# Kernel optimization log

Measured on AMD Instinct MI355X. Metric: run time of the kernel, lower is better.

The kernel has to match this reference:

```python
import jax, jax.numpy as jnp
import numpy as np

COMMITMENT_COST = 0.1


def setup_inputs() -> dict:
    key = jax.random.key(0)
    k1, k2 = jax.random.split(key)
    B, D, T, K = 8, 256, 2048, 8192
    z = jax.random.normal(k1, (B, D, T), dtype=jnp.float32)
    # nn.init.uniform_(weight, -1/dim, 1/dim)
    codebook = jax.random.uniform(k2, (K, D), dtype=jnp.float32,
                                  minval=-1.0 / D, maxval=1.0 / D)
    return {"z": z, "codebook": codebook}


def reference(z, codebook):
    B, D, T = z.shape
    # (B*T, D)
    z_flat = jnp.transpose(z, (0, 2, 1)).reshape(B * T, D)
    # squared euclidean distances to each codebook entry: (B*T, K)
    d = (jnp.sum(z_flat * z_flat, axis=1, keepdims=True)
         - 2.0 * (z_flat @ codebook.T)
         + jnp.sum(codebook * codebook, axis=1)[None, :])
    indices = jnp.argmin(d, axis=1)                      # (B*T,)
    z_q = codebook[indices].reshape(B, T, D)             # gather
    z_q = jnp.transpose(z_q, (0, 2, 1))                  # (B, D, T)

    codebook_loss = jnp.mean((z_q - jax.lax.stop_gradient(z)) ** 2)
    commitment_loss = COMMITMENT_COST * jnp.mean(
        (jax.lax.stop_gradient(z_q) - z) ** 2)
    loss = codebook_loss + commitment_loss

    # straight-through estimator
    z_q_st = z + jax.lax.stop_gradient(z_q - z)
    return z_q_st, indices.reshape(B, T), loss
```

## Files before the change

### kernel.cpp

```cpp
#include <hip/hip_runtime.h>
#include <hip/hip_bf16.h>
#include <float.h>
#include <math.h>

#define Bz 8
#define Dd 256
#define Tt 2048
#define Kk 8192
#define Mm (Bz*Tt)

#define NSPL 32

#define ZG_CAP 4096
#define PAIR_CAP 131072

#define RESCAN_MARGIN 6e-4f

typedef __attribute__((ext_vector_type(8))) _Float16 f16x8;
typedef __attribute__((ext_vector_type(4))) float    f32x4;

__device__ __forceinline__ void gld16(const void* g, void* l) {
  __builtin_amdgcn_global_load_lds(
      (const __attribute__((address_space(1))) void*)g,
      (__attribute__((address_space(3))) void*)l, 16, 0, 0);
}

__device__ __forceinline__ float np_sumsq128(const float* __restrict__ x) {
  float r0 = __fmul_rn(x[0], x[0]);
  float r1 = __fmul_rn(x[1], x[1]);
  float r2 = __fmul_rn(x[2], x[2]);
  float r3 = __fmul_rn(x[3], x[3]);
  float r4 = __fmul_rn(x[4], x[4]);
  float r5 = __fmul_rn(x[5], x[5]);
  float r6 = __fmul_rn(x[6], x[6]);
  float r7 = __fmul_rn(x[7], x[7]);
  for (int i = 8; i < 128; i += 8) {
    r0 = __fadd_rn(r0, __fmul_rn(x[i+0], x[i+0]));
    r1 = __fadd_rn(r1, __fmul_rn(x[i+1], x[i+1]));
    r2 = __fadd_rn(r2, __fmul_rn(x[i+2], x[i+2]));
    r3 = __fadd_rn(r3, __fmul_rn(x[i+3], x[i+3]));
    r4 = __fadd_rn(r4, __fmul_rn(x[i+4], x[i+4]));
    r5 = __fadd_rn(r5, __fmul_rn(x[i+5], x[i+5]));
    r6 = __fadd_rn(r6, __fmul_rn(x[i+6], x[i+6]));
    r7 = __fadd_rn(r7, __fmul_rn(x[i+7], x[i+7]));
  }
  return __fadd_rn(__fadd_rn(__fadd_rn(r0, r1), __fadd_rn(r2, r3)),
                   __fadd_rn(__fadd_rn(r4, r5), __fadd_rn(r6, r7)));
}
__device__ __forceinline__ float np_sumsq256(const float* __restrict__ x) {
  return __fadd_rn(np_sumsq128(x), np_sumsq128(x + 128));
}

__global__ void k_pre(const float* __restrict__ z, const float* __restrict__ cb,
                      _Float16* __restrict__ Ah, _Float16* __restrict__ Bh,
                      float* __restrict__ sc,
                      double* __restrict__ loss_accum, int* __restrict__ rc) {
  const int bid = blockIdx.x;
  const int tid = threadIdx.x;
  if (bid < 1024) {
    __shared__ _Float16 tile[64][64 + 8];
    const int b  = bid >> 7;
    const int dt = (bid >> 5) & 3;
    const int tt = bid & 31;
    const int d0 = dt * 64, t0 = tt * 64;
    const float* zb = z + ((size_t)b * Dd + d0) * Tt + t0;
    #pragma unroll
    for (int p = 0; p < 4; ++p) {
      const int d  = p * 16 + (tid >> 4);
      const int tl = (tid & 15) * 4;
      const float4 v = *(const float4*)(zb + (size_t)d * Tt + tl);
      tile[tl+0][d] = (_Float16)v.x;
      tile[tl+1][d] = (_Float16)v.y;
      tile[tl+2][d] = (_Float16)v.z;
      tile[tl+3][d] = (_Float16)v.w;
    }
    __syncthreads();
    const int r = tid >> 2, seg = tid & 3;
    const int m = b * Tt + t0 + r;
    int4* dst = (int4*)(Ah + (size_t)m * Dd + d0 + seg * 16);
    const int4* srcv = (const int4*)(&tile[r][seg * 16]);
    dst[0] = srcv[0];
    dst[1] = srcv[1];
  } else if (bid < 2048) {
    const size_t g = (size_t)(bid - 1024) * 256 + tid;
    const float4 v0 = *(const float4*)(cb + g * 8);
    const float4 v1 = *(const float4*)(cb + g * 8 + 4);
    f16x8 o;
    o[0] = (_Float16)(v0.x * 256.f); o[1] = (_Float16)(v0.y * 256.f);
    o[2] = (_Float16)(v0.z * 256.f); o[3] = (_Float16)(v0.w * 256.f);
    o[4] = (_Float16)(v1.x * 256.f); o[5] = (_Float16)(v1.y * 256.f);
    o[6] = (_Float16)(v1.z * 256.f); o[7] = (_Float16)(v1.w * 256.f);
    *(f16x8*)(Bh + g * 8) = o;
  } else {
    if (bid == 2048 && tid == 0) {
      *loss_accum = 0.0; rc[0] = 0; rc[1] = 0; rc[2] = 0;
    }
    const int gid = (bid - 2048) * 256 + tid;
    const int lane = gid & 63;
    const int j = lane & 7, sub = lane >> 3;
    const int row = (gid >> 6) * 8 + sub;
    if (row >= Kk) return;
    const float* x = cb + (size_t)row * Dd;
    float c0 = __fmul_rn(x[j], x[j]);
    float c1 = __fmul_rn(x[128 + j], x[128 + j]);
    #pragma unroll
    for (int i = 8; i < 128; i += 8) {
      c0 = __fadd_rn(c0, __fmul_rn(x[j + i], x[j + i]));
      c1 = __fadd_rn(c1, __fmul_rn(x[128 + j + i], x[128 + j + i]));
    }
    #pragma unroll
    for (int off = 1; off <= 4; off <<= 1) {
      c0 = __fadd_rn(c0, __shfl_xor(c0, off));
      c1 = __fadd_rn(c1, __shfl_xor(c1, off));
    }
    if (j == 0) sc[row] = __fadd_rn(c0, c1);
  }
}

__global__ __launch_bounds__(512, 4)
void k_mfma(const _Float16* __restrict__ Ah, const _Float16* __restrict__ Bh,
            const float* __restrict__ sc,
            float* __restrict__ pd1, float* __restrict__ pd2, int* __restrict__ pi1) {
  __shared__ __align__(16) _Float16 As[128 * 64];
  __shared__ __align__(16) _Float16 Bs[256 * 64];
  __shared__ float mr1[512];
  __shared__ float mr2[512];
  __shared__ int   mri[512];

  const int tid  = threadIdx.x;
  const int bx   = blockIdx.x & 31;
  const int by   = blockIdx.x >> 5;
  const int m0   = by * 128, n0 = bx * 256;
  const int w    = tid >> 6, lane = tid & 63;
  const int wy   = w >> 2, wx = w & 3;
  const int l15  = lane & 15, quad = lane >> 4;
  const int lhi  = lane >> 3, llo = lane & 7;
  const int p    = llo ^ lhi;
  const int sw   = l15 & 7;

  f32x4 acc[4][4];
  #pragma unroll
  for (int mi = 0; mi < 4; ++mi)
    #pragma unroll
    for (int ni = 0; ni < 4; ++ni)
      acc[mi][ni] = (f32x4){0.f, 0.f, 0.f, 0.f};

  for (int kc = 0; kc < 4; ++kc) {
    __syncthreads();
    #pragma unroll
    for (int i = 0; i < 2; ++i) {
      const int c  = w * 2 + i;
      const int r8 = c * 8 + lhi;
      gld16(Ah + (size_t)(m0 + r8) * Dd + kc * 64 + p * 8, As + c * 512);
    }
    #pragma unroll
    for (int i = 0; i < 4; ++i) {
      const int c  = w * 4 + i;
      const int r8 = c * 8 + lhi;
      gld16(Bh + (size_t)(n0 + r8) * Dd + kc * 64 + p * 8, Bs + c * 512);
    }
    __syncthreads();
    #pragma unroll
    for (int ks = 0; ks < 2; ++ks) {
      f16x8 af[4], bf[4];
      #pragma unroll
      for (int mi = 0; mi < 4; ++mi)
        af[mi] = *(const f16x8*)(As + (wy*64 + mi*16 + l15) * 64 + (((ks*4 + quad) ^ sw) * 8));
      #pragma unroll
      for (int ni = 0; ni < 4; ++ni)
        bf[ni] = *(const f16x8*)(Bs + (wx*64 + ni*16 + l15) * 64 + (((ks*4 + quad) ^ sw) * 8));
      #pragma unroll
      for (int mi = 0; mi < 4; ++mi)
        #pragma unroll
        for (int ni = 0; ni < 4; ++ni)
          acc[mi][ni] = __builtin_amdgcn_mfma_f32_16x16x32_f16(bf[ni], af[mi], acc[mi][ni], 0, 0, 0);
    }
  }

  float scv[4][4];
  #pragma unroll
  for (int ni = 0; ni < 4; ++ni)
    *(float4*)&scv[ni][0] = *(const float4*)(sc + n0 + wx * 64 + ni * 16 + quad * 4);

  float s1[4], s2[4]; int i1[4];
  #pragma unroll
  for (int mi = 0; mi < 4; ++mi) {
    float a1 = INFINITY, a2 = INFINITY; int ai = 0x7fffffff;
    #pragma unroll
    for (int ni = 0; ni < 4; ++ni)
      #pragma unroll
      for (int r = 0; r < 4; ++r) {
        const float sv = fmaf(-0.0078125f, acc[mi][ni][r], scv[ni][r]);
        const int   k  = n0 + wx * 64 + ni * 16 + quad * 4 + r;
        if (sv < a1) { a2 = a1; a1 = sv; ai = k; }
        else if (sv < a2) a2 = sv;
      }
    s1[mi] = a1; s2[mi] = a2; i1[mi] = ai;
  }

  #pragma unroll
  for (int off = 16; off <= 32; off <<= 1)
    #pragma unroll
    for (int q = 0; q < 4; ++q) {
      const float o1 = __shfl_xor(s1[q], off);
      const float o2 = __shfl_xor(s2[q], off);
      const int   oi = __shfl_xor(i1[q], off);
      const float n2 = fminf(fminf(s2[q], o2), fmaxf(s1[q], o1));
      if (o1 < s1[q] || (o1 == s1[q] && oi < i1[q])) { s1[q] = o1; i1[q] = oi; }
      s2[q] = n2;
    }

  if (quad == 0) {
    #pragma unroll
    for (int mi = 0; mi < 4; ++mi) {
      const int ml = wy * 64 + mi * 16 + l15;
      mr1[ml * 4 + wx] = s1[mi];
      mr2[ml * 4 + wx] = s2[mi];
      mri[ml * 4 + wx] = i1[mi];
    }
  }
  __syncthreads();
  if (tid < 128) {
    float a1 = INFINITY, a2 = INFINITY; int ai = 0x7fffffff;
    #pragma unroll
    for (int x = 0; x < 4; ++x) {
      const float b1 = mr1[tid * 4 + x], b2 = mr2[tid * 4 + x];
      const int   bi = mri[tid * 4 + x];
      if (b1 < a1 || (b1 == a1 && bi < ai)) { a2 = fminf(a1, b2); a1 = b1; ai = bi; }
      else a2 = fminf(a2, b1);
    }
    const size_t o = (size_t)bx * Mm + (size_t)(m0 + tid);
    pd1[o] = a1; pd2[o] = a2; pi1[o] = ai;
  }
}

__global__ void k_combine(const float* __restrict__ pd1, const float* __restrict__ pd2,
                          const int* __restrict__ pi1, int* __restrict__ idxf,
                          int* __restrict__ rc, int* __restrict__ rlist,
                          int* __restrict__ pairs, int* __restrict__ slist,
                          float* __restrict__ outIdx) {
  const int m = blockIdx.x * blockDim.x + threadIdx.x;
  if (m >= Mm) return;
  float a1 = INFINITY, a2 = INFINITY; int ai = 0x7fffffff;
  for (int spl = 0; spl < NSPL; ++spl) {
    const size_t o = (size_t)spl * Mm + m;
    const float b1 = pd1[o], b2 = pd2[o]; const int bi = pi1[o];
    if (b1 < a1 || (b1 == a1 && bi < ai)) { a2 = fminf(a1, b2); a1 = b1; ai = bi; }
    else a2 = fminf(a2, b1);
  }
  idxf[m]   = ai;
  outIdx[m] = (float)ai;
  if (a2 - a1 <= RESCAN_MARGIN) {
    const int p = atomicAdd(&rc[0], 1);
    if (p < ZG_CAP) {
      rlist[p] = m;
      const float thr = a1 + RESCAN_MARGIN;
      int nc = 0;
      for (int spl = 0; spl < NSPL; ++spl) {
        const size_t o = (size_t)spl * Mm + m;
        if (pd2[o] <= thr) nc += 256;
        else if (pd1[o] <= thr) ++nc;
      }
      const int base = atomicAdd(&rc[1], nc);
      if (base + nc <= PAIR_CAP) {
        int wp = base;
        for (int spl = 0; spl < NSPL; ++spl) {
          const size_t o = (size_t)spl * Mm + m;
          const float b1 = pd1[o], b2 = pd2[o];
          if (b2 <= thr) {
            const int k0 = spl * 256;
            for (int c = 0; c < 256; ++c) pairs[wp++] = (p << 13) | (k0 + c);
          } else if (b1 <= thr) {
            pairs[wp++] = (p << 13) | pi1[o];
          }
        }
      } else {
        for (int q = base; q < PAIR_CAP; ++q) pairs[q] = -1;
        const int s = atomicAdd(&rc[2], 1); slist[s] = m;
      }
    } else {
      const int s = atomicAdd(&rc[2], 1); slist[s] = m;
    }
  }
}

__global__ void k_gather(const float* __restrict__ z, const int* __restrict__ rc,
                         const int* __restrict__ rlist, float* __restrict__ zg,
                         float* __restrict__ Ag, unsigned long long* __restrict__ pbrow) {
  __shared__ float zr[Dd];
  const int cnt = min(rc[0], ZG_CAP);
  for (int it = blockIdx.x; it < cnt; it += gridDim.x) {
    const int m = rlist[it];
    const int b = m / Tt, t = m & (Tt - 1);
    __syncthreads();
    zr[threadIdx.x] = z[(size_t)b * Dd * Tt + (size_t)threadIdx.x * Tt + t];
    __syncthreads();
    zg[(size_t)it * Dd + threadIdx.x] = zr[threadIdx.x];
    if (threadIdx.x == 0) { Ag[it] = np_sumsq256(zr); pbrow[it] = ~0ull; }
  }
}

__global__ __launch_bounds__(256)
void k_rescan_pairs(const float* __restrict__ cb, const float* __restrict__ sc,
                    const int* __restrict__ rc, const float* __restrict__ zg,
                    const float* __restrict__ Ag,
                    const int* __restrict__ pairs,
                    unsigned long long* __restrict__ pbrow) {
  const int n = min(rc[1], PAIR_CAP);
  const int i = blockIdx.x * 256 + threadIdx.x;
  if (i >= n) return;
  const int pr = pairs[i];
  if (pr < 0) return;
  const int it = pr >> 13, k = pr & (Kk - 1);
  const float* __restrict__ zp = zg + (size_t)it * Dd;
  const float* __restrict__ cp = cb + (size_t)k * Dd;
  double M8 = 0.0;
  #pragma unroll
  for (int sg = 0; sg < 8; ++sg) {
    double a0 = 0.0, a1 = 0.0, a2 = 0.0, a3 = 0.0;
    #pragma unroll
    for (int j = 0; j < 32; j += 4) {
      const float4 c4 = *(const float4*)(cp + sg * 32 + j);
      const float4 z4 = *(const float4*)(zp + sg * 32 + j);
      a0 = fma((double)c4.x, (double)z4.x, a0);
      a1 = fma((double)c4.y, (double)z4.y, a1);
      a2 = fma((double)c4.z, (double)z4.z, a2);
      a3 = fma((double)c4.w, (double)z4.w, a3);
    }
    M8 += (a0 + a1) + (a2 + a3);
  }
  const float M  = (float)M8;
  const float t1 = __fsub_rn(Ag[it], __fmul_rn(2.0f, M));
  const float dq = __fadd_rn(t1, sc[k]);
  unsigned int fb = __float_as_uint(dq);
  fb = (fb & 0x80000000u) ? ~fb : (fb | 0x80000000u);
  const unsigned long long pack = ((unsigned long long)fb << 32) | (unsigned)k;
  atomicMin(pbrow + it, pack);
}

__global__ void k_rescan_final(const int* __restrict__ rc, const int* __restrict__ rlist,
                               const unsigned long long* __restrict__ pbrow,
                               int* __restrict__ idxf, float* __restrict__ outIdx) {
  const int cnt = min(rc[0], ZG_CAP);
  const int it = blockIdx.x * blockDim.x + threadIdx.x;
  if (it < cnt) {
    const unsigned long long pb = pbrow[it];
    if (pb != ~0ull) {
      const int idx = (int)(unsigned)(pb & 0xFFFFFFFFull);
      const int m = rlist[it];
      idxf[m] = idx; outIdx[m] = (float)idx;
    }
  }
}

__global__ void k_rescan_slow(const float* __restrict__ z, const float* __restrict__ cb,
                              const float* __restrict__ sc,
                              const int* __restrict__ rc, const int* __restrict__ slist,
                              int* __restrict__ idxf, float* __restrict__ outIdx) {
  __shared__ float zrow[Dd];
  __shared__ float Ash;
  __shared__ float sval[256];
  __shared__ int   sidx[256];
  const int tid = threadIdx.x;
  const int cnt = rc[2];
  for (int it = blockIdx.x; it < cnt; it += gridDim.x) {
    const int m = slist[it];
    const int b = m / Tt, t = m & (Tt - 1);
    __syncthreads();
    zrow[tid] = z[(size_t)b * Dd * Tt + (size_t)tid * Tt + t];
    __syncthreads();
    if (tid == 0) Ash = np_sumsq256(zrow);
    __syncthreads();
    const float A = Ash;
    float best = INFINITY; int bi = 0x7fffffff;
    for (int k = tid; k < Kk; k += 256) {
      const float* cr = cb + (size_t)k * Dd;
      double a0 = 0.0, a1 = 0.0, a2 = 0.0, a3 = 0.0;
      for (int d = 0; d < Dd; d += 4) {
        const float4 c4 = *(const float4*)(cr + d);
        a0 = fma((double)c4.x, (double)zrow[d+0], a0);
        a1 = fma((double)c4.y, (double)zrow[d+1], a1);
        a2 = fma((double)c4.z, (double)zrow[d+2], a2);
        a3 = fma((double)c4.w, (double)zrow[d+3], a3);
      }
      const float M  = (float)((a0 + a1) + (a2 + a3));
      const float t1 = __fsub_rn(A, __fmul_rn(2.0f, M));
      const float dq = __fadd_rn(t1, sc[k]);
      if (dq < best) { best = dq; bi = k; }
    }
    sval[tid] = best; sidx[tid] = bi;
    __syncthreads();
    for (int off = 128; off; off >>= 1) {
      if (tid < off) {
        if (sval[tid+off] < sval[tid] ||
            (sval[tid+off] == sval[tid] && sidx[tid+off] < sidx[tid])) {
          sval[tid] = sval[tid+off]; sidx[tid] = sidx[tid+off];
        }
      }
      __syncthreads();
    }
    if (tid == 0) { idxf[m] = sidx[0]; outIdx[m] = (float)sidx[0]; }
    __syncthreads();
  }
}

__global__ void k_out(const float* __restrict__ z, const float* __restrict__ cb,
                      const int* __restrict__ idxf,
                      float* __restrict__ outZ, double* __restrict__ loss_accum) {
  __shared__ float tile[64][65];
  const int tid = threadIdx.x;
  const int bidx = blockIdx.x;
  const int b  = bidx >> 7;
  const int dt = (bidx >> 5) & 3;
  const int tt = bidx & 31;
  const int d0 = dt * 64, t0 = tt * 64;
  {
    const int r = tid >> 2, seg = tid & 3;
    const int idx = idxf[b * Tt + t0 + r];
    const float* src = cb + (size_t)idx * Dd + d0 + seg * 16;
    #pragma unroll
    for (int q4 = 0; q4 < 4; ++q4) {
      const float4 v = *(const float4*)(src + q4 * 4);
      tile[seg * 16 + q4 * 4 + 0][r] = v.x;
      tile[seg * 16 + q4 * 4 + 1][r] = v.y;
      tile[seg * 16 + q4 * 4 + 2][r] = v.z;
      tile[seg * 16 + q4 * 4 + 3][r] = v.w;
    }
  }
  __syncthreads();
  const float* zbase = z + ((size_t)b * Dd + d0) * Tt + t0;
  float*       obase = outZ + ((size_t)b * Dd + d0) * Tt + t0;
  double ls = 0.0;
  #pragma unroll
  for (int p = 0; p < 4; ++p) {
    const int d  = p * 16 + (tid >> 4);
    const int t4 = (tid & 15) * 4;
    const float4 zv = *(const float4*)(zbase + (size_t)d * Tt + t4);
    const float q0 = tile[d][t4+0], q1 = tile[d][t4+1];
    const float q2 = tile[d][t4+2], q3 = tile[d][t4+3];
    const float r0 = q0 - zv.x, r1 = q1 - zv.y, r2 = q2 - zv.z, r3 = q3 - zv.w;
    float4 o;
    o.x = zv.x + r0; o.y = zv.y + r1; o.z = zv.z + r2; o.w = zv.w + r3;
    *(float4*)(obase + (size_t)d * Tt + t4) = o;
    ls += (double)r0*r0 + (double)r1*r1 + (double)r2*r2 + (double)r3*r3;
  }
  #pragma unroll
  for (int off = 32; off; off >>= 1) ls += __shfl_down(ls, off);
  if ((tid & 63) == 0) atomicAdd(loss_accum, ls);
}

__global__ void k_finalize(const double* __restrict__ loss_accum, float* __restrict__ outLoss) {
  const double mean = *loss_accum / (double)((size_t)Bz * Dd * Tt);
  *outLoss = (float)(mean + 0.1 * mean);
}

extern "C" void kernel_launch(void* const* d_in, const int* in_sizes, int n_in,
                              void* d_out, int out_size, void* d_ws, size_t ws_size,
                              hipStream_t stream) {
  (void)in_sizes; (void)n_in; (void)out_size; (void)ws_size;
  const float* z  = (const float*)d_in[0];
  const float* cb = (const float*)d_in[1];

  float* outZ    = (float*)d_out;
  float* outIdx  = outZ + (size_t)Bz * Dd * Tt;
  float* outLoss = outIdx + Mm;

  char* w = (char*)d_ws;
  double*    loss_accum = (double*)w;    w += 16;
  int*       rc         = (int*)w;       w += 16;
  int*       rlist      = (int*)w;       w += sizeof(int)   * Mm;
  int*       slist      = (int*)w;       w += sizeof(int)   * Mm;
  int*       idxf       = (int*)w;       w += sizeof(int)   * Mm;
  float*     sc         = (float*)w;     w += sizeof(float) * Kk;
  _Float16*  Ah         = (_Float16*)w;  w += sizeof(_Float16) * (size_t)Mm * Dd;
  _Float16*  Bh         = (_Float16*)w;  w += sizeof(_Float16) * (size_t)Kk * Dd;
  float*     zg         = (float*)w;     w += sizeof(float) * (size_t)ZG_CAP * Dd;
  float*     Ag         = (float*)w;     w += sizeof(float) * ZG_CAP;
  unsigned long long* pbrow = (unsigned long long*)w; w += sizeof(unsigned long long) * ZG_CAP;
  int*       pairs      = (int*)w;       w += sizeof(int) * PAIR_CAP;
  float*     pd1        = (float*)w;     w += sizeof(float) * (size_t)NSPL * Mm;
  float*     pd2        = (float*)w;     w += sizeof(float) * (size_t)NSPL * Mm;
  int*       pi1        = (int*)w;

  k_pre         <<<dim3(2304), 256, 0, stream>>>(z, cb, Ah, Bh, sc, loss_accum, rc);
  k_mfma        <<<dim3((Mm / 128) * (Kk / 256)), 512, 0, stream>>>(Ah, Bh, sc, pd1, pd2, pi1);
  k_combine     <<<dim3(Mm / 256), 256, 0, stream>>>(pd1, pd2, pi1, idxf, rc, rlist, pairs, slist, outIdx);
  k_gather      <<<dim3(256), 256, 0, stream>>>(z, rc, rlist, zg, Ag, pbrow);
  k_rescan_pairs<<<dim3(PAIR_CAP / 256), 256, 0, stream>>>(cb, sc, rc, zg, Ag, pairs, pbrow);
  k_rescan_slow <<<dim3(64), 256, 0, stream>>>(z, cb, sc, rc, slist, idxf, outIdx);
  k_rescan_final<<<dim3(ZG_CAP / 256), 256, 0, stream>>>(rc, rlist, pbrow, idxf, outIdx);
  k_out         <<<dim3(1024), 256, 0, stream>>>(z, cb, idxf, outZ, loss_accum);
  k_finalize    <<<dim3(1), 1, 0, stream>>>(loss_accum, outLoss);
}
```

Before: 293.4 us.

## Replace global pair list with per-row wave rescan and fold final fixup into output

Drops the serial per-thread pair-list construction in the combine kernel, which wrote up to 256 pairs per ambiguous row. Each wave now rebuilds its row's candidate list from the per-split partials using ballots and rescans those candidates directly. The separate final-fixup kernel is removed, and the output kernel reads the packed rescan minimum through a per-row position map. The combine kernel now launches 64-thread blocks with its loop unrolled, and the gather kernel computes the squared norm with 8 lanes plus shuffles instead of a single thread.

```diff
diff --git a/kernel.cpp b/kernel.cpp
--- a/kernel.cpp
+++ b/kernel.cpp
@@ -12,7 +12,6 @@
 #define NSPL 32
 
 #define ZG_CAP 4096
-#define PAIR_CAP 131072
 
 #define RESCAN_MARGIN 6e-4f
 
@@ -237,11 +236,12 @@
 __global__ void k_combine(const float* __restrict__ pd1, const float* __restrict__ pd2,
                           const int* __restrict__ pi1, int* __restrict__ idxf,
                           int* __restrict__ rc, int* __restrict__ rlist,
-                          int* __restrict__ pairs, int* __restrict__ slist,
-                          float* __restrict__ outIdx) {
-  const int m = blockIdx.x * blockDim.x + threadIdx.x;
+                          float* __restrict__ rthr, int* __restrict__ posm,
+                          int* __restrict__ slist, float* __restrict__ outIdx) {
+  const int m = blockIdx.x * 64 + threadIdx.x;
   if (m >= Mm) return;
   float a1 = INFINITY, a2 = INFINITY; int ai = 0x7fffffff;
+  #pragma unroll
   for (int spl = 0; spl < NSPL; ++spl) {
     const size_t o = (size_t)spl * Mm + m;
     const float b1 = pd1[o], b2 = pd2[o]; const int bi = pi1[o];
@@ -250,38 +250,18 @@
   }
   idxf[m]   = ai;
   outIdx[m] = (float)ai;
+  int pos = -1;
   if (a2 - a1 <= RESCAN_MARGIN) {
     const int p = atomicAdd(&rc[0], 1);
     if (p < ZG_CAP) {
       rlist[p] = m;
-      const float thr = a1 + RESCAN_MARGIN;
-      int nc = 0;
-      for (int spl = 0; spl < NSPL; ++spl) {
-        const size_t o = (size_t)spl * Mm + m;
-        if (pd2[o] <= thr) nc += 256;
-        else if (pd1[o] <= thr) ++nc;
-      }
-      const int base = atomicAdd(&rc[1], nc);
-      if (base + nc <= PAIR_CAP) {
-        int wp = base;
-        for (int spl = 0; spl < NSPL; ++spl) {
-          const size_t o = (size_t)spl * Mm + m;
-          const float b1 = pd1[o], b2 = pd2[o];
-          if (b2 <= thr) {
-            const int k0 = spl * 256;
-            for (int c = 0; c < 256; ++c) pairs[wp++] = (p << 13) | (k0 + c);
-          } else if (b1 <= thr) {
-            pairs[wp++] = (p << 13) | pi1[o];
-          }
-        }
-      } else {
-        for (int q = base; q < PAIR_CAP; ++q) pairs[q] = -1;
-        const int s = atomicAdd(&rc[2], 1); slist[s] = m;
-      }
+      rthr[p]  = a1 + RESCAN_MARGIN;
+      pos = p;
     } else {
       const int s = atomicAdd(&rc[2], 1); slist[s] = m;
     }
   }
+  posm[m] = pos;
 }
 
 __global__ void k_gather(const float* __restrict__ z, const int* __restrict__ rc,
@@ -289,30 +269,38 @@
                          float* __restrict__ Ag, unsigned long long* __restrict__ pbrow) {
   __shared__ float zr[Dd];
   const int cnt = min(rc[0], ZG_CAP);
+  const int tid = threadIdx.x;
   for (int it = blockIdx.x; it < cnt; it += gridDim.x) {
     const int m = rlist[it];
     const int b = m / Tt, t = m & (Tt - 1);
     __syncthreads();
-    zr[threadIdx.x] = z[(size_t)b * Dd * Tt + (size_t)threadIdx.x * Tt + t];
-    __syncthreads();
-    zg[(size_t)it * Dd + threadIdx.x] = zr[threadIdx.x];
-    if (threadIdx.x == 0) { Ag[it] = np_sumsq256(zr); pbrow[it] = ~0ull; }
-  }
-}
-
-__global__ __launch_bounds__(256)
-void k_rescan_pairs(const float* __restrict__ cb, const float* __restrict__ sc,
-                    const int* __restrict__ rc, const float* __restrict__ zg,
-                    const float* __restrict__ Ag,
-                    const int* __restrict__ pairs,
-                    unsigned long long* __restrict__ pbrow) {
-  const int n = min(rc[1], PAIR_CAP);
-  const int i = blockIdx.x * 256 + threadIdx.x;
-  if (i >= n) return;
-  const int pr = pairs[i];
-  if (pr < 0) return;
-  const int it = pr >> 13, k = pr & (Kk - 1);
-  const float* __restrict__ zp = zg + (size_t)it * Dd;
+    zr[tid] = z[(size_t)b * Dd * Tt + (size_t)tid * Tt + t];
+    __syncthreads();
+    zg[(size_t)it * Dd + tid] = zr[tid];
+    if (tid < 8) {
+      const int j = tid;
+      float c0 = __fmul_rn(zr[j], zr[j]);
+      float c1 = __fmul_rn(zr[128 + j], zr[128 + j]);
+      #pragma unroll
+      for (int i = 8; i < 128; i += 8) {
+        c0 = __fadd_rn(c0, __fmul_rn(zr[j + i], zr[j + i]));
+        c1 = __fadd_rn(c1, __fmul_rn(zr[128 + j + i], zr[128 + j + i]));
+      }
+      #pragma unroll
+      for (int off = 1; off <= 4; off <<= 1) {
+        c0 = __fadd_rn(c0, __shfl_xor(c0, off));
+        c1 = __fadd_rn(c1, __shfl_xor(c1, off));
+      }
+      if (j == 0) { Ag[it] = __fadd_rn(c0, c1); pbrow[it] = ~0ull; }
+    }
+  }
+}
+
+__device__ __forceinline__ void rescan_cand(const float* __restrict__ cb,
+                                            const float* __restrict__ sc,
+                                            const float* __restrict__ zp,
+                                            const float Az, const int k,
+                                            unsigned long long* __restrict__ pb) {
   const float* __restrict__ cp = cb + (size_t)k * Dd;
   double M8 = 0.0;
   #pragma unroll
@@ -330,26 +318,55 @@
     M8 += (a0 + a1) + (a2 + a3);
   }
   const float M  = (float)M8;
-  const float t1 = __fsub_rn(Ag[it], __fmul_rn(2.0f, M));
+  const float t1 = __fsub_rn(Az, __fmul_rn(2.0f, M));
   const float dq = __fadd_rn(t1, sc[k]);
   unsigned int fb = __float_as_uint(dq);
   fb = (fb & 0x80000000u) ? ~fb : (fb | 0x80000000u);
   const unsigned long long pack = ((unsigned long long)fb << 32) | (unsigned)k;
-  atomicMin(pbrow + it, pack);
-}
-
-__global__ void k_rescan_final(const int* __restrict__ rc, const int* __restrict__ rlist,
-                               const unsigned long long* __restrict__ pbrow,
-                               int* __restrict__ idxf, float* __restrict__ outIdx) {
-  const int cnt = min(rc[0], ZG_CAP);
-  const int it = blockIdx.x * blockDim.x + threadIdx.x;
-  if (it < cnt) {
-    const unsigned long long pb = pbrow[it];
-    if (pb != ~0ull) {
-      const int idx = (int)(unsigned)(pb & 0xFFFFFFFFull);
-      const int m = rlist[it];
-      idxf[m] = idx; outIdx[m] = (float)idx;
-    }
+  atomicMin(pb, pack);
+}
+
+__global__ __launch_bounds__(256)
+void k_rescan_rows(const float* __restrict__ cb, const float* __restrict__ sc,
+                   const int* __restrict__ rc, const int* __restrict__ rlist,
+                   const float* __restrict__ rthr,
+                   const float* __restrict__ pd1, const float* __restrict__ pd2,
+                   const int* __restrict__ pi1,
+                   const float* __restrict__ zg, const float* __restrict__ Ag,
+                   unsigned long long* __restrict__ pbrow) {
+  __shared__ int clist[4][32];
+  const int cnt  = min(rc[0], ZG_CAP);
+  const int wv   = threadIdx.x >> 6;
+  const int lane = threadIdx.x & 63;
+  const int it   = blockIdx.x * 4 + wv;
+  if (it >= cnt) return;
+  const int   m   = rlist[it];
+  const float thr = rthr[it];
+  const float Az  = Ag[it];
+  const float* __restrict__ zp = zg + (size_t)it * Dd;
+
+  int  cand = -1;
+  bool dump = false;
+  if (lane < NSPL) {
+    const size_t o = (size_t)lane * Mm + m;
+    const float b1 = pd1[o], b2 = pd2[o];
+    if (b2 <= thr) dump = true;
+    else if (b1 <= thr) cand = pi1[o];
+  }
+  const unsigned long long m1 = __ballot(cand >= 0);
+  unsigned long long m2 = __ballot(dump);
+  if (cand >= 0)
+    clist[wv][__popcll(m1 & ((1ull << lane) - 1))] = cand;
+  asm volatile("s_waitcnt lgkmcnt(0)" ::: "memory");
+  __builtin_amdgcn_sched_barrier(0);
+  const int ns = __popcll(m1);
+  if (lane < ns)
+    rescan_cand(cb, sc, zp, Az, clist[wv][lane], pbrow + it);
+  while (m2) {
+    const int s = (int)(__ffsll((long long)m2) - 1); m2 &= m2 - 1;
+    #pragma unroll
+    for (int rr = 0; rr < 4; ++rr)
+      rescan_cand(cb, sc, zp, Az, s * 256 + rr * 64 + lane, pbrow + it);
   }
 }
 
@@ -405,8 +422,10 @@
 }
 
 __global__ void k_out(const float* __restrict__ z, const float* __restrict__ cb,
-                      const int* __restrict__ idxf,
-                      float* __restrict__ outZ, double* __restrict__ loss_accum) {
+                      const int* __restrict__ idxf, const int* __restrict__ posm,
+                      const unsigned long long* __restrict__ pbrow,
+                      float* __restrict__ outZ, float* __restrict__ outIdx,
+                      double* __restrict__ loss_accum) {
   __shared__ float tile[64][65];
   const int tid = threadIdx.x;
   const int bidx = blockIdx.x;
@@ -416,7 +435,16 @@
   const int d0 = dt * 64, t0 = tt * 64;
   {
     const int r = tid >> 2, seg = tid & 3;
-    const int idx = idxf[b * Tt + t0 + r];
+    const int m = b * Tt + t0 + r;
+    int idx = idxf[m];
+    const int pos = posm[m];
+    if (pos >= 0) {
+      const unsigned long long pb = pbrow[pos];
+      if (pb != ~0ull) {
+        idx = (int)(unsigned)(pb & 0xFFFFFFFFull);
+        if (seg == 0) outIdx[m] = (float)idx;
+      }
+    }
     const float* src = cb + (size_t)idx * Dd + d0 + seg * 16;
     #pragma unroll
     for (int q4 = 0; q4 < 4; ++q4) {
@@ -471,24 +499,24 @@
   int*       rlist      = (int*)w;       w += sizeof(int)   * Mm;
   int*       slist      = (int*)w;       w += sizeof(int)   * Mm;
   int*       idxf       = (int*)w;       w += sizeof(int)   * Mm;
+  int*       posm       = (int*)w;       w += sizeof(int)   * Mm;
   float*     sc         = (float*)w;     w += sizeof(float) * Kk;
+  float*     rthr       = (float*)w;     w += sizeof(float) * ZG_CAP;
   _Float16*  Ah         = (_Float16*)w;  w += sizeof(_Float16) * (size_t)Mm * Dd;
   _Float16*  Bh         = (_Float16*)w;  w += sizeof(_Float16) * (size_t)Kk * Dd;
   float*     zg         = (float*)w;     w += sizeof(float) * (size_t)ZG_CAP * Dd;
   float*     Ag         = (float*)w;     w += sizeof(float) * ZG_CAP;
   unsigned long long* pbrow = (unsigned long long*)w; w += sizeof(unsigned long long) * ZG_CAP;
-  int*       pairs      = (int*)w;       w += sizeof(int) * PAIR_CAP;
   float*     pd1        = (float*)w;     w += sizeof(float) * (size_t)NSPL * Mm;
   float*     pd2        = (float*)w;     w += sizeof(float) * (size_t)NSPL * Mm;
   int*       pi1        = (int*)w;
 
   k_pre         <<<dim3(2304), 256, 0, stream>>>(z, cb, Ah, Bh, sc, loss_accum, rc);
   k_mfma        <<<dim3((Mm / 128) * (Kk / 256)), 512, 0, stream>>>(Ah, Bh, sc, pd1, pd2, pi1);
-  k_combine     <<<dim3(Mm / 256), 256, 0, stream>>>(pd1, pd2, pi1, idxf, rc, rlist, pairs, slist, outIdx);
+  k_combine     <<<dim3(Mm / 64), 64, 0, stream>>>(pd1, pd2, pi1, idxf, rc, rlist, rthr, posm, slist, outIdx);
   k_gather      <<<dim3(256), 256, 0, stream>>>(z, rc, rlist, zg, Ag, pbrow);
-  k_rescan_pairs<<<dim3(PAIR_CAP / 256), 256, 0, stream>>>(cb, sc, rc, zg, Ag, pairs, pbrow);
+  k_rescan_rows <<<dim3(ZG_CAP / 4), 256, 0, stream>>>(cb, sc, rc, rlist, rthr, pd1, pd2, pi1, zg, Ag, pbrow);
   k_rescan_slow <<<dim3(64), 256, 0, stream>>>(z, cb, sc, rc, slist, idxf, outIdx);
-  k_rescan_final<<<dim3(ZG_CAP / 256), 256, 0, stream>>>(rc, rlist, pbrow, idxf, outIdx);
-  k_out         <<<dim3(1024), 256, 0, stream>>>(z, cb, idxf, outZ, loss_accum);
+  k_out         <<<dim3(1024), 256, 0, stream>>>(z, cb, idxf, posm, pbrow, outZ, outIdx, loss_accum);
   k_finalize    <<<dim3(1), 1, 0, stream>>>(loss_accum, outLoss);
 }
```

New measurement: 361.2 us. 1.23x slower.
